# Kernel tuning notes

Measured on AMD Instinct MI355X. Metric: run time of the kernel, lower is better.

The kernel has to match this reference:

```python
import jax, jax.numpy as jnp
import numpy as np

D_MODEL = 1024
NUM_HEADS = 16
D_K = D_MODEL // NUM_HEADS
CLAMP = 1e9
EPS = 1e-12


def setup_inputs() -> dict:
    key = jax.random.key(0)
    ks = jax.random.split(key, 11)
    B, S, D = 4, 2048, D_MODEL
    std = 1.0 / np.sqrt(D)
    inp = {
        'Q': jax.random.normal(ks[0], (B, S, D), jnp.float32),
        'K': jax.random.normal(ks[1], (B, S, D), jnp.float32),
        'V': jax.random.normal(ks[2], (B, S, D), jnp.float32),
        'Wq': jax.random.normal(ks[3], (D, D), jnp.float32) * std,
        'bq': jnp.zeros((D,), jnp.float32),
        'Wk': jax.random.normal(ks[4], (D, D), jnp.float32) * std,
        'bk': jnp.zeros((D,), jnp.float32),
        'Wv': jax.random.normal(ks[5], (D, D), jnp.float32) * std,
        'bv': jnp.zeros((D,), jnp.float32),
        'Wo': jax.random.normal(ks[6], (D, D), jnp.float32) * std,
        'bo': jnp.zeros((D,), jnp.float32),
    }
    return inp


def _split_heads(x):
    b, s, _ = x.shape
    return x.reshape(b, s, NUM_HEADS, D_K).transpose(0, 2, 1, 3)  # [b,h,s,dk]


def reference(Q, K, V, Wq, bq, Wk, bk, Wv, bv, Wo, bo):
    Qh = _split_heads(Q @ Wq.T + bq)
    Kh = _split_heads(K @ Wk.T + bk)
    Vh = _split_heads(V @ Wv.T + bv)
    scale = jnp.sqrt(jnp.asarray(D_K, Qh.dtype))
    scores = jnp.einsum('bhqd,bhkd->bhqk', Qh, Kh) / scale
    scores = scores - jnp.max(scores, axis=-1, keepdims=True)
    scores = jnp.clip(scores, -CLAMP, CLAMP)
    attn = jax.nn.softmax(scores, axis=-1)
    attn = jnp.clip(attn, EPS, None)
    attn = attn / jnp.sum(attn, axis=-1, keepdims=True)
    ctx = jnp.einsum('bhqk,bhkd->bhqd', attn, Vh)
    b, h, s, dk = ctx.shape
    ctx = ctx.transpose(0, 2, 1, 3).reshape(b, s, D_MODEL)
    return ctx @ Wo.T + bo
```

## Files before the change

kernel.cpp:

```cpp
#include <hip/hip_runtime.h>
#include <hip/hip_bf16.h>


typedef float  f32x4  __attribute__((ext_vector_type(4)));
typedef __bf16 bf16x8 __attribute__((ext_vector_type(8)));
typedef short  s16x8  __attribute__((ext_vector_type(8)));
typedef int    i32x4  __attribute__((ext_vector_type(4)));

#define MFMA16(a,b,c) __builtin_amdgcn_mfma_f32_16x16x32_bf16((a),(b),(c),0,0,0)

__device__ __forceinline__ unsigned short f2bf(float f) {
    union { float f; unsigned u; } v; v.f = f;
    unsigned r = v.u + 0x7fffu + ((v.u >> 16) & 1u);
    return (unsigned short)(r >> 16);
}

__device__ __forceinline__ float exp2_fast(float x) {
    float r;
    asm("v_exp_f32 %0, %1" : "=v"(r) : "v"(x));
    return r;
}

__device__ __forceinline__ int cvtpk_bf16(float lo, float hi) {
    int r;
    asm("v_cvt_pk_bf16_f32 %0, %1, %2" : "=v"(r) : "v"(lo), "v"(hi));
    return r;
}
__device__ __forceinline__ s16x8 pk8(f32x4 x, f32x4 y) {
    i32x4 r;
    r[0] = cvtpk_bf16(x[0], x[1]);
    r[1] = cvtpk_bf16(x[2], x[3]);
    r[2] = cvtpk_bf16(y[0], y[1]);
    r[3] = cvtpk_bf16(y[2], y[3]);
    return __builtin_bit_cast(s16x8, r);
}
__device__ __forceinline__ void plswap32(int& a, int& b) {
    asm("v_permlane32_swap_b32 %0, %1" : "+v"(a), "+v"(b));
}
__device__ __forceinline__ void plswap16(int& a, int& b) {
    asm("v_permlane16_swap_b32 %0, %1" : "+v"(a), "+v"(b));
}

__device__ __forceinline__ void pack_pf(const f32x4 pe[4], bf16x8& pf0, bf16x8& pf1) {
    int a0 = cvtpk_bf16(pe[0][0], pe[0][1]);
    int a1 = cvtpk_bf16(pe[0][2], pe[0][3]);
    int b0 = cvtpk_bf16(pe[1][0], pe[1][1]);
    int b1 = cvtpk_bf16(pe[1][2], pe[1][3]);
    plswap32(a0, b0); plswap32(a1, b1);
    plswap16(a0, b0); plswap16(a1, b1);
    i32x4 f0; f0[0] = a0; f0[1] = a1; f0[2] = b0; f0[3] = b1;
    int c0 = cvtpk_bf16(pe[2][0], pe[2][1]);
    int c1 = cvtpk_bf16(pe[2][2], pe[2][3]);
    int d0 = cvtpk_bf16(pe[3][0], pe[3][1]);
    int d1 = cvtpk_bf16(pe[3][2], pe[3][3]);
    plswap32(c0, d0); plswap32(c1, d1);
    plswap16(c0, d0); plswap16(c1, d1);
    i32x4 f1; f1[0] = c0; f1[1] = c1; f1[2] = d0; f1[3] = d1;
    pf0 = __builtin_bit_cast(bf16x8, f0);
    pf1 = __builtin_bit_cast(bf16x8, f1);
}

__global__ __launch_bounds__(256) void proj_kernel(
    const float* __restrict__ Qf, const float* __restrict__ Kf,
    const float* __restrict__ Vf,
    const float* __restrict__ Wqf, const float* __restrict__ Wkf,
    const float* __restrict__ Wvf,
    const float* __restrict__ bqf, const float* __restrict__ bkf,
    const float* __restrict__ bvf,
    unsigned short* __restrict__ Qh, unsigned short* __restrict__ Kh,
    unsigned short* __restrict__ Vtw, float qscale)
{
    constexpr int K = 1024;
    __shared__ unsigned short Ash[128 * 32];
    __shared__ unsigned short Bsh[128 * 32];

    const int t    = threadIdx.x;
    const int w    = t >> 6;
    const int lane = t & 63;
    const int wm   = w >> 1, wn = w & 1;
    const int lr   = lane & 15, quad = lane >> 4;

    const int z = blockIdx.z;
    const float *Af, *Wf, *bias;
    float scale;
    unsigned short* out;
    if (z == 0)      { Af = Qf;  Wf = Wqf; bias = bqf; out = Qh;  scale = qscale; }
    else if (z == 1) { Af = Kf;  Wf = Wkf; bias = bkf; out = Kh;  scale = 1.0f; }
    else             { Af = Wvf; Wf = Vf;  bias = bvf; out = Vtw; scale = 1.0f; }

    int m0, n0;
    if (z < 2) {
        m0 = (blockIdx.x * 8 + (blockIdx.y >> 3)) * 128;
        n0 = (blockIdx.y & 7) * 128;
    } else {
        m0 = (blockIdx.y & 7) * 128;
        n0 = (blockIdx.x * 8 + (blockIdx.y >> 3)) * 128;
    }

    const int srow = t >> 2;
    const int skp  = (t & 3) * 8;

    const float* Ap0 = Af + (size_t)(m0 + srow) * K + skp;
    const float* Ap1 = Ap0 + (size_t)64 * K;
    const float* Wp0 = Wf + (size_t)(n0 + srow) * K + skp;
    const float* Wp1 = Wp0 + (size_t)64 * K;
    unsigned short* dA = &Ash[srow * 32 + skp];
    unsigned short* dB = &Bsh[srow * 32 + skp];

    f32x4 a0x, a0y, a1x, a1y, w0x, w0y, w1x, w1y;
#define LOADP(kk) do {                                                        \
        a0x = *(const f32x4*)(Ap0 + (kk)); a0y = *(const f32x4*)(Ap0 + (kk) + 4); \
        a1x = *(const f32x4*)(Ap1 + (kk)); a1y = *(const f32x4*)(Ap1 + (kk) + 4); \
        w0x = *(const f32x4*)(Wp0 + (kk)); w0y = *(const f32x4*)(Wp0 + (kk) + 4); \
        w1x = *(const f32x4*)(Wp1 + (kk)); w1y = *(const f32x4*)(Wp1 + (kk) + 4); \
    } while (0)

    f32x4 acc[4][4] = {};
    LOADP(0);

    for (int k0 = 0; k0 < K; k0 += 32) {
        __syncthreads();
        *(s16x8*)dA              = pk8(a0x, a0y);
        *(s16x8*)(dA + 64 * 32)  = pk8(a1x, a1y);
        *(s16x8*)dB              = pk8(w0x, w0y);
        *(s16x8*)(dB + 64 * 32)  = pk8(w1x, w1y);
        const int kn = (k0 + 32) & 1023;
        LOADP(kn);
        __syncthreads();

        bf16x8 af[4], bw[4];
#pragma unroll
        for (int i = 0; i < 4; i++)
            af[i] = *(const bf16x8*)&Ash[(wm * 64 + i * 16 + lr) * 32 + quad * 8];
#pragma unroll
        for (int j = 0; j < 4; j++)
            bw[j] = *(const bf16x8*)&Bsh[(wn * 64 + j * 16 + lr) * 32 + quad * 8];

#pragma unroll
        for (int i = 0; i < 4; i++)
#pragma unroll
            for (int j = 0; j < 4; j++)
                acc[i][j] = MFMA16(af[i], bw[j], acc[i][j]);
    }
#undef LOADP

#pragma unroll
    for (int i = 0; i < 4; i++) {
#pragma unroll
        for (int j = 0; j < 4; j++) {
            const int n = n0 + wn * 64 + j * 16 + lr;
#pragma unroll
            for (int r = 0; r < 4; r++) {
                const int m = m0 + wm * 64 + i * 16 + quad * 4 + r;
                float val = (acc[i][j][r] + ((z == 2) ? bias[m] : bias[n])) * scale;
                if (z < 2) {
                    const int b = m >> 11, s = m & 2047, h = n >> 6, d = n & 63;
                    out[(((size_t)(b * 16 + h) * 2048 + s) << 6) + d] = f2bf(val);
                } else {
                    const int h = m >> 6, d = m & 63, b = n >> 11, s = n & 2047;
                    out[((size_t)(b * 16 + h) * 64 + d) * 2048 + s] = f2bf(val);
                }
            }
        }
    }
}

__global__ __launch_bounds__(256) void gemm_o(
    const unsigned short* __restrict__ A,
    const float* __restrict__ Wf,
    const float* __restrict__ bias,
    float* __restrict__ out)
{
    constexpr int K = 1024;
    __shared__ unsigned short Ash[128 * 32];
    __shared__ unsigned short Bsh[128 * 32];

    const int t    = threadIdx.x;
    const int w    = t >> 6;
    const int lane = t & 63;
    const int wm   = w >> 1, wn = w & 1;
    const int lr   = lane & 15, quad = lane >> 4;

    const int m0 = (blockIdx.x * 8 + (blockIdx.y >> 3)) * 128;
    const int n0 = (blockIdx.y & 7) * 128;

    const int srow = t >> 2;
    const int skp  = (t & 3) * 8;

    const unsigned short* Ap0 = A + (size_t)(m0 + srow) * K + skp;
    const unsigned short* Ap1 = Ap0 + (size_t)64 * K;
    const float* Wp0 = Wf + (size_t)(n0 + srow) * K + skp;
    const float* Wp1 = Wp0 + (size_t)64 * K;
    unsigned short* dA = &Ash[srow * 32 + skp];
    unsigned short* dB = &Bsh[srow * 32 + skp];

    s16x8 av0, av1;
    f32x4 w0x, w0y, w1x, w1y;
#define LOADO(kk) do {                                                        \
        av0 = *(const s16x8*)(Ap0 + (kk));                                    \
        av1 = *(const s16x8*)(Ap1 + (kk));                                    \
        w0x = *(const f32x4*)(Wp0 + (kk)); w0y = *(const f32x4*)(Wp0 + (kk) + 4); \
        w1x = *(const f32x4*)(Wp1 + (kk)); w1y = *(const f32x4*)(Wp1 + (kk) + 4); \
    } while (0)

    f32x4 acc[4][4] = {};
    LOADO(0);

    for (int k0 = 0; k0 < K; k0 += 32) {
        __syncthreads();
        *(s16x8*)dA             = av0;
        *(s16x8*)(dA + 64 * 32) = av1;
        *(s16x8*)dB             = pk8(w0x, w0y);
        *(s16x8*)(dB + 64 * 32) = pk8(w1x, w1y);
        const int kn = (k0 + 32) & 1023;
        LOADO(kn);
        __syncthreads();

        bf16x8 af[4], bw[4];
#pragma unroll
        for (int i = 0; i < 4; i++)
            af[i] = *(const bf16x8*)&Ash[(wm * 64 + i * 16 + lr) * 32 + quad * 8];
#pragma unroll
        for (int j = 0; j < 4; j++)
            bw[j] = *(const bf16x8*)&Bsh[(wn * 64 + j * 16 + lr) * 32 + quad * 8];

#pragma unroll
        for (int i = 0; i < 4; i++)
#pragma unroll
            for (int j = 0; j < 4; j++)
                acc[i][j] = MFMA16(af[i], bw[j], acc[i][j]);
    }
#undef LOADO

#pragma unroll
    for (int i = 0; i < 4; i++) {
#pragma unroll
        for (int j = 0; j < 4; j++) {
            const int n = n0 + wn * 64 + j * 16 + lr;
#pragma unroll
            for (int r = 0; r < 4; r++) {
                const int m = m0 + wm * 64 + i * 16 + quad * 4 + r;
                out[(size_t)m * 1024 + n] = acc[i][j][r] + bias[n];
            }
        }
    }
}

__global__ __launch_bounds__(256) void attn_kernel(
    const unsigned short* __restrict__ Qh,
    const unsigned short* __restrict__ Kh,
    const unsigned short* __restrict__ Vt,
    unsigned short* __restrict__ ctx)
{
    constexpr int KS = 72;
    __shared__ unsigned short Ksh[64 * KS];
    __shared__ unsigned short Vts[64 * KS];

    const int t    = threadIdx.x;
    const int w    = t >> 6;
    const int lane = t & 63;
    const int lr   = lane & 15, quad = lane >> 4;

    const int bh = blockIdx.y, qblk = blockIdx.x;
    const size_t base = (size_t)bh * 2048 * 64;
    const unsigned short* Qp = Qh + base;
    const unsigned short* Kg = Kh + base + (size_t)lane * 64 + w * 16;
    const unsigned short* Vg = Vt + base + (size_t)lane * 2048 + w * 16;

    const int q0 = qblk * 128 + w * 32;
    const unsigned short* qr0 = Qp + (size_t)(q0 + lr) * 64;
    const unsigned short* qr1 = Qp + (size_t)(q0 + 16 + lr) * 64;
    bf16x8 aq0 = *(const bf16x8*)(qr0 + quad * 8);
    bf16x8 aq1 = *(const bf16x8*)(qr0 + 32 + quad * 8);
    bf16x8 aq2 = *(const bf16x8*)(qr1 + quad * 8);
    bf16x8 aq3 = *(const bf16x8*)(qr1 + 32 + quad * 8);

    f32x4 Of0[4] = {}, Of1[4] = {};
    float ls0 = 0.f, ls1 = 0.f;

    s16x8 kv0 = *(const s16x8*)(Kg);
    s16x8 kv1 = *(const s16x8*)(Kg + 8);
    s16x8 vv0 = *(const s16x8*)(Vg);
    s16x8 vv1 = *(const s16x8*)(Vg + 8);

    for (int kb = 0; kb < 2048; kb += 64) {
        __syncthreads();
        *(s16x8*)&Ksh[lane * KS + w * 16]     = kv0;
        *(s16x8*)&Ksh[lane * KS + w * 16 + 8] = kv1;
        *(s16x8*)&Vts[lane * KS + w * 16]     = vv0;
        *(s16x8*)&Vts[lane * KS + w * 16 + 8] = vv1;

        const int kn = (kb + 64) & 2047;
        kv0 = *(const s16x8*)(Kg + (size_t)kn * 64);
        kv1 = *(const s16x8*)(Kg + (size_t)kn * 64 + 8);
        vv0 = *(const s16x8*)(Vg + kn);
        vv1 = *(const s16x8*)(Vg + kn + 8);

        __syncthreads();

        f32x4 pe0[4], pe1[4];
#pragma unroll
        for (int nt = 0; nt < 4; nt++) {
            const unsigned short* kr = &Ksh[(16 * nt + lr) * KS + quad * 8];
            bf16x8 k0 = *(const bf16x8*)kr;
            bf16x8 k1 = *(const bf16x8*)(kr + 32);
            f32x4 c0 = {}, c1 = {};
            c0 = MFMA16(k0, aq0, c0); c0 = MFMA16(k1, aq1, c0);
            c1 = MFMA16(k0, aq2, c1); c1 = MFMA16(k1, aq3, c1);
            f32x4 p0, p1;
#pragma unroll
            for (int r = 0; r < 4; r++) p0[r] = exp2_fast(c0[r]);
#pragma unroll
            for (int r = 0; r < 4; r++) p1[r] = exp2_fast(c1[r]);
            ls0 += (p0[0] + p0[1]) + (p0[2] + p0[3]);
            ls1 += (p1[0] + p1[1]) + (p1[2] + p1[3]);
            pe0[nt] = p0; pe1[nt] = p1;
        }

        bf16x8 pf00, pf01, pf10, pf11;
        pack_pf(pe0, pf00, pf01);
        pack_pf(pe1, pf10, pf11);

#pragma unroll
        for (int dt = 0; dt < 4; dt++) {
            const unsigned short* vr = &Vts[(dt * 16 + lr) * KS + quad * 8];
            bf16x8 v0 = *(const bf16x8*)vr;
            bf16x8 v1 = *(const bf16x8*)(vr + 32);
            Of0[dt] = MFMA16(pf00, v0, Of0[dt]);
            Of0[dt] = MFMA16(pf01, v1, Of0[dt]);
            Of1[dt] = MFMA16(pf10, v0, Of1[dt]);
            Of1[dt] = MFMA16(pf11, v1, Of1[dt]);
        }
    }

    ls0 += __shfl_xor(ls0, 16);
    ls0 += __shfl_xor(ls0, 32);
    ls1 += __shfl_xor(ls1, 16);
    ls1 += __shfl_xor(ls1, 32);

    const int b = bh >> 4, h = bh & 15;
#pragma unroll
    for (int r = 0; r < 4; r++) {
        const float inv0 = 1.0f / __shfl(ls0, quad * 4 + r, 64);
        const int qa = q0 + quad * 4 + r;
        unsigned short* cp0 = ctx + ((size_t)b * 2048 + qa) * 1024 + h * 64;
#pragma unroll
        for (int dt = 0; dt < 4; dt++)
            cp0[dt * 16 + lr] = f2bf(Of0[dt][r] * inv0);

        const float inv1 = 1.0f / __shfl(ls1, quad * 4 + r, 64);
        const int qb = q0 + 16 + quad * 4 + r;
        unsigned short* cp1 = ctx + ((size_t)b * 2048 + qb) * 1024 + h * 64;
#pragma unroll
        for (int dt = 0; dt < 4; dt++)
            cp1[dt * 16 + lr] = f2bf(Of1[dt][r] * inv1);
    }
}

extern "C" void kernel_launch(void* const* d_in, const int* in_sizes, int n_in,
                              void* d_out, int out_size, void* d_ws, size_t ws_size,
                              hipStream_t stream) {
    const float* Q  = (const float*)d_in[0];
    const float* K  = (const float*)d_in[1];
    const float* V  = (const float*)d_in[2];
    const float* Wq = (const float*)d_in[3];
    const float* bq = (const float*)d_in[4];
    const float* Wk = (const float*)d_in[5];
    const float* bk = (const float*)d_in[6];
    const float* Wv = (const float*)d_in[7];
    const float* bv = (const float*)d_in[8];
    const float* Wo = (const float*)d_in[9];
    const float* bo = (const float*)d_in[10];

    const size_t EB = (size_t)8192 * 1024;
    unsigned short* Qh  = (unsigned short*)d_ws;
    unsigned short* Kh  = Qh  + EB;
    unsigned short* Vtw = Kh  + EB;
    unsigned short* Ctx = Vtw + EB;

    const float QSCALE = 0.125f * 1.44269504088896340736f;

    dim3 tb(256);
    proj_kernel<<<dim3(8, 64, 3), tb, 0, stream>>>(
        Q, K, V, Wq, Wk, Wv, bq, bk, bv, Qh, Kh, Vtw, QSCALE);
    attn_kernel<<<dim3(16, 64), tb, 0, stream>>>(Qh, Kh, Vtw, Ctx);
    gemm_o<<<dim3(8, 64), tb, 0, stream>>>(Ctx, Wo, bo, (float*)d_out);
}
```

Measured before the change: 384.4 us.

## Pre-convert Wo to bf16 and double-buffer output GEMM via direct global-to-LDS loads

Adds a small kernel that converts Wo to bf16 in workspace before the pipeline, so the output projection GEMM reads bf16 weights directly. gemm_o now uses global_load_lds to stream A and W tiles straight into double-buffered shared memory, with explicit vmcnt waits and barriers in place of register staging and repacking. It also remaps block indices for a different tile traversal order. The cost is an extra kernel launch, extra workspace, and twice the LDS per block, which may lower occupancy.

```diff
diff --git a/kernel.cpp b/kernel.cpp
--- a/kernel.cpp
+++ b/kernel.cpp
@@ -13,6 +13,23 @@
     union { float f; unsigned u; } v; v.f = f;
     unsigned r = v.u + 0x7fffu + ((v.u >> 16) & 1u);
     return (unsigned short)(r >> 16);
+}
+
+__device__ __forceinline__ s16x8 cvt8(const float* __restrict__ p) {
+    f32x4 x = *(const f32x4*)p;
+    f32x4 y = *(const f32x4*)(p + 4);
+    s16x8 r;
+    r[0] = (short)f2bf(x[0]); r[1] = (short)f2bf(x[1]);
+    r[2] = (short)f2bf(x[2]); r[3] = (short)f2bf(x[3]);
+    r[4] = (short)f2bf(y[0]); r[5] = (short)f2bf(y[1]);
+    r[6] = (short)f2bf(y[2]); r[7] = (short)f2bf(y[3]);
+    return r;
+}
+
+__device__ __forceinline__ void gl_lds16(const void* g, void* l) {
+    __builtin_amdgcn_global_load_lds(
+        (const __attribute__((address_space(1))) unsigned int*)g,
+        (__attribute__((address_space(3))) unsigned int*)l, 16, 0, 0);
 }
 
 __device__ __forceinline__ float exp2_fast(float x) {
@@ -60,6 +77,13 @@
     pf1 = __builtin_bit_cast(bf16x8, f1);
 }
 
+__global__ __launch_bounds__(256) void cvt_kernel(
+    const float* __restrict__ src, unsigned short* __restrict__ dst, int n8)
+{
+    int i = blockIdx.x * 256 + threadIdx.x;
+    if (i < n8) *(s16x8*)(dst + (size_t)i * 8) = cvt8(src + (size_t)i * 8);
+}
+
 __global__ __launch_bounds__(256) void proj_kernel(
     const float* __restrict__ Qf, const float* __restrict__ Kf,
     const float* __restrict__ Vf,
@@ -167,13 +191,13 @@
 
 __global__ __launch_bounds__(256) void gemm_o(
     const unsigned short* __restrict__ A,
-    const float* __restrict__ Wf,
+    const unsigned short* __restrict__ W,
     const float* __restrict__ bias,
     float* __restrict__ out)
 {
     constexpr int K = 1024;
-    __shared__ unsigned short Ash[128 * 32];
-    __shared__ unsigned short Bsh[128 * 32];
+    __shared__ unsigned short Ash[2 * 128 * 32];
+    __shared__ unsigned short Bsh[2 * 128 * 32];
 
     const int t    = threadIdx.x;
     const int w    = t >> 6;
@@ -181,56 +205,64 @@
     const int wm   = w >> 1, wn = w & 1;
     const int lr   = lane & 15, quad = lane >> 4;
 
-    const int m0 = (blockIdx.x * 8 + (blockIdx.y >> 3)) * 128;
-    const int n0 = (blockIdx.y & 7) * 128;
+    const int bid  = blockIdx.y * 8 + blockIdx.x;
+    const int orig = (bid & 7) * 64 + (bid >> 3);
+    const int n0 = (orig & 7) * 128;
+    const int m0 = (orig >> 3) * 128;
 
     const int srow = t >> 2;
     const int skp  = (t & 3) * 8;
 
     const unsigned short* Ap0 = A + (size_t)(m0 + srow) * K + skp;
     const unsigned short* Ap1 = Ap0 + (size_t)64 * K;
-    const float* Wp0 = Wf + (size_t)(n0 + srow) * K + skp;
-    const float* Wp1 = Wp0 + (size_t)64 * K;
-    unsigned short* dA = &Ash[srow * 32 + skp];
-    unsigned short* dB = &Bsh[srow * 32 + skp];
-
-    s16x8 av0, av1;
-    f32x4 w0x, w0y, w1x, w1y;
-#define LOADO(kk) do {                                                        \
-        av0 = *(const s16x8*)(Ap0 + (kk));                                    \
-        av1 = *(const s16x8*)(Ap1 + (kk));                                    \
-        w0x = *(const f32x4*)(Wp0 + (kk)); w0y = *(const f32x4*)(Wp0 + (kk) + 4); \
-        w1x = *(const f32x4*)(Wp1 + (kk)); w1y = *(const f32x4*)(Wp1 + (kk) + 4); \
+    const unsigned short* Wp0 = W + (size_t)(n0 + srow) * K + skp;
+    const unsigned short* Wp1 = Wp0 + (size_t)64 * K;
+    unsigned short* lA0 = &Ash[w * 512];
+    unsigned short* lA1 = &Ash[2048 + w * 512];
+    unsigned short* lB0 = &Bsh[w * 512];
+    unsigned short* lB1 = &Bsh[2048 + w * 512];
+
+#define STAGE(buf, k0) do {                       \
+        gl_lds16(Ap0 + (k0), lA0 + (buf) * 4096); \
+        gl_lds16(Ap1 + (k0), lA1 + (buf) * 4096); \
+        gl_lds16(Wp0 + (k0), lB0 + (buf) * 4096); \
+        gl_lds16(Wp1 + (k0), lB1 + (buf) * 4096); \
     } while (0)
 
     f32x4 acc[4][4] = {};
-    LOADO(0);
+
+    STAGE(0, 0);
+    int cur = 0;
 
     for (int k0 = 0; k0 < K; k0 += 32) {
-        __syncthreads();
-        *(s16x8*)dA             = av0;
-        *(s16x8*)(dA + 64 * 32) = av1;
-        *(s16x8*)dB             = pk8(w0x, w0y);
-        *(s16x8*)(dB + 64 * 32) = pk8(w1x, w1y);
-        const int kn = (k0 + 32) & 1023;
-        LOADO(kn);
-        __syncthreads();
+        if (k0 + 32 < K) {
+            STAGE(cur ^ 1, k0 + 32);
+            asm volatile("s_waitcnt vmcnt(4)" ::: "memory");
+        } else {
+            asm volatile("s_waitcnt vmcnt(0)" ::: "memory");
+        }
+        __builtin_amdgcn_s_barrier();
+        __builtin_amdgcn_sched_barrier(0);
 
         bf16x8 af[4], bw[4];
 #pragma unroll
         for (int i = 0; i < 4; i++)
-            af[i] = *(const bf16x8*)&Ash[(wm * 64 + i * 16 + lr) * 32 + quad * 8];
+            af[i] = *(const bf16x8*)&Ash[cur * 4096 + (wm * 64 + i * 16 + lr) * 32 + quad * 8];
 #pragma unroll
         for (int j = 0; j < 4; j++)
-            bw[j] = *(const bf16x8*)&Bsh[(wn * 64 + j * 16 + lr) * 32 + quad * 8];
+            bw[j] = *(const bf16x8*)&Bsh[cur * 4096 + (wn * 64 + j * 16 + lr) * 32 + quad * 8];
 
 #pragma unroll
         for (int i = 0; i < 4; i++)
 #pragma unroll
             for (int j = 0; j < 4; j++)
                 acc[i][j] = MFMA16(af[i], bw[j], acc[i][j]);
-    }
-#undef LOADO
+
+        __builtin_amdgcn_sched_barrier(0);
+        __builtin_amdgcn_s_barrier();
+        cur ^= 1;
+    }
+#undef STAGE
 
 #pragma unroll
     for (int i = 0; i < 4; i++) {
@@ -373,16 +405,19 @@
     const float* bo = (const float*)d_in[10];
 
     const size_t EB = (size_t)8192 * 1024;
+    const size_t EW = (size_t)1024 * 1024;
     unsigned short* Qh  = (unsigned short*)d_ws;
     unsigned short* Kh  = Qh  + EB;
     unsigned short* Vtw = Kh  + EB;
     unsigned short* Ctx = Vtw + EB;
+    unsigned short* Wob = Ctx + EB;
 
     const float QSCALE = 0.125f * 1.44269504088896340736f;
 
     dim3 tb(256);
+    cvt_kernel<<<(int)(EW / 8 / 256), tb, 0, stream>>>(Wo, Wob, (int)(EW / 8));
     proj_kernel<<<dim3(8, 64, 3), tb, 0, stream>>>(
         Q, K, V, Wq, Wk, Wv, bq, bk, bv, Qh, Kh, Vtw, QSCALE);
     attn_kernel<<<dim3(16, 64), tb, 0, stream>>>(Qh, Kh, Vtw, Ctx);
-    gemm_o<<<dim3(8, 64), tb, 0, stream>>>(Ctx, Wo, bo, (float*)d_out);
-}
+    gemm_o<<<dim3(8, 64), tb, 0, stream>>>(Ctx, Wob, bo, (float*)d_out);
+}
```

After: 377.5 us. Within noise of the previous version (-1.8%).
